# Performance work log

Measured on AMD Instinct MI355X. Metric: run time of the kernel, lower is better.

## Reference

```python
import jax, jax.numpy as jnp
import numpy as np

N_ATOMS = 64
N_SAMPLES = 2 ** 15
SAMPLERATE = 22050
N_RES = 4096
N_ROOMS = 8
N_COEFFS = N_SAMPLES // 2 + 1


def make_waves():
    # musical_scale_hz(21, 106, 4096//4) -> 4 waveform families (sine, saw, square, triangle)
    n_steps = N_RES // 4
    midi = np.linspace(21.0, 106.0, n_steps)
    f0 = 440.0 * 2.0 ** ((midi - 69.0) / 12.0)
    rps = ((f0 / (SAMPLERATE / 2.0)) * np.pi).astype(np.float32)
    rad = rps[:, None] * np.arange(N_SAMPLES, dtype=np.float32)[None, :]
    sine = np.sin(rad)
    t = rad / (2.0 * np.pi)
    saw = (2.0 * (t - np.floor(t + 0.5))).astype(np.float32)
    sq = np.sign(sine).astype(np.float32)
    tri = (2.0 * np.abs(saw) - 1.0).astype(np.float32)
    return jnp.asarray(np.concatenate([sine, saw, sq, tri], 0).reshape(1, N_RES, N_SAMPLES))


def pdf2(means, stds, n):
    # gaussian pdf evaluated on linspace(0,1,n); means/stds: (1, A)
    rng = jnp.linspace(0.0, 1.0, n)
    mu = means[..., None]
    sd = stds[..., None]
    return jnp.exp(-0.5 * ((rng - mu) / sd) ** 2) / (sd * jnp.sqrt(2.0 * jnp.pi))


def linear_interp(x, n_out):
    # F.interpolate(mode='linear', align_corners=False) on last axis; x: (b, a, f)
    f = x.shape[-1]
    pos = (jnp.arange(n_out) + 0.5) * (f / n_out) - 0.5
    pos = jnp.clip(pos, 0.0, f - 1)
    i0 = jnp.floor(pos).astype(jnp.int32)
    i1 = jnp.minimum(i0 + 1, f - 1)
    w = (pos - i0).astype(x.dtype)
    return x[..., i0] * (1.0 - w) + x[..., i1] * w


def exponential_decay(decay_values, n_atoms, n_frames, base_resonance, n_samples):
    dv = jax.nn.sigmoid(decay_values.reshape(-1, n_atoms, 1))
    dv = jnp.broadcast_to(dv, (dv.shape[0], n_atoms, n_frames))
    decay = base_resonance + dv * (1.0 - base_resonance) * 0.95
    decay = jnp.exp(jnp.cumsum(jnp.log(decay + 1e-12), axis=-1))
    return linear_interp(decay, n_samples)


def fft_convolve(a, b):
    # zero-pad to 2N, multiply spectra, take first N samples
    n = a.shape[-1]
    pa = jnp.pad(a, ((0, 0), (0, 0), (0, n)))
    pb = jnp.pad(b, ((0, 0), (0, 0), (0, n)))
    spec = jnp.fft.rfft(pa, axis=-1) * jnp.fft.rfft(pb, axis=-1)
    return jnp.fft.irfft(spec, n=2 * n, axis=-1)[..., :n]


def layer_norm(x, w, b, eps=1e-5):
    m = jnp.mean(x, axis=-1, keepdims=True)
    v = jnp.var(x, axis=-1, keepdims=True)
    return (x - m) / jnp.sqrt(v + eps) * w + b


def sparse_softmax_st(x):
    soft = jax.nn.softmax(x, axis=-1)
    hard = jax.nn.one_hot(jnp.argmax(x, axis=-1), x.shape[-1], dtype=x.dtype)
    return hard + soft - jax.lax.stop_gradient(soft)


def model_forward(x, mix, decays, filter_decays, resonance_choice, noise_filter,
                  resonance_filter, resonance_filter2, env, amplitudes, verb_params,
                  noise, waves, ln_w, ln_b, mix_w1, mix_w2, room_w1, room_w2, room_irs):
    overall_mix = jax.nn.softmax(mix, axis=-1)                                   # (1,A,2)
    resonances = jnp.einsum('bar,brn->ban', jax.nn.relu(resonance_choice), waves)  # (1,A,N)

    # band-pass filtered noise (gaussian filter in frequency domain)
    noise_spec = jnp.fft.rfft(noise, axis=-1)
    noise_filt = pdf2(noise_filter[:, :, 0], jnp.abs(noise_filter[:, :, 1]) + 1e-12, N_COEFFS)
    filtered_noise = jnp.fft.irfft(noise_spec * noise_filt, n=N_SAMPLES, axis=-1)

    res_spec = jnp.fft.rfft(resonances, axis=-1)
    rf1 = pdf2(jnp.zeros_like(resonance_filter[:, :, 0]),
               jnp.abs(resonance_filter[:, :, 1]) + 1e-12, N_COEFFS)
    filtered_resonance = jnp.fft.irfft(res_spec * rf1, n=N_SAMPLES, axis=-1)
    rf2 = pdf2(jnp.zeros_like(resonance_filter2[:, :, 0]),
               jnp.abs(resonance_filter2[:, :, 1]) + 1e-12, N_COEFFS)
    filt_res_2 = jnp.fft.irfft(res_spec * rf2, n=N_SAMPLES, axis=-1)

    filt_crossfade = exponential_decay(filter_decays, N_ATOMS, 128, 0.02, N_SAMPLES)
    decay_env = exponential_decay(decays, N_ATOMS, 128, 0.02, N_SAMPLES)
    decaying_resonance = filtered_resonance * decay_env
    decaying_resonance2 = filt_res_2 * decay_env

    # gaussian envelope branch (gaussian_envelope = True)
    envelopes = pdf2(env[:, :, 0], jnp.abs(env[:, :, 1] + 1e-12) * 0.1, N_SAMPLES)
    positioned_noise = filtered_noise * envelopes

    res = fft_convolve(positioned_noise, decaying_resonance)
    res2 = fft_convolve(positioned_noise, decaying_resonance2)
    mixed = filt_crossfade * res + (1.0 - filt_crossfade) * res2

    final = positioned_noise * overall_mix[:, :, 0:1] + mixed * overall_mix[:, :, 1:2]
    final = final / (jnp.linalg.norm(final, axis=-1, keepdims=True) + 1e-8)
    amps = jnp.abs(amplitudes)
    final = final * amps

    # ReverbGenerator: layernorm -> small MLPs -> hard room choice -> fft convolve with IR
    h = layer_norm(verb_params, ln_w, ln_b)
    mix_v = jax.nn.sigmoid(jax.nn.leaky_relu(h @ mix_w1) @ mix_w2)               # (1,A,1)
    room_logits = jax.nn.leaky_relu(h @ room_w1) @ room_w2                        # (1,A,R)
    room = sparse_softmax_st(room_logits)
    ir = jnp.einsum('bar,rn->ban', room, room_irs)
    wet = fft_convolve(final, ir)
    out = final * mix_v + wet * (1.0 - mix_v)
    return out, amps


def setup_inputs() -> dict:
    key = jax.random.key(0)
    ks = jax.random.split(key, 20)
    return {
        'x': jax.random.normal(ks[0], (1, 1), jnp.float32),
        'mix': jax.random.uniform(ks[1], (1, N_ATOMS, 2), jnp.float32),
        'decays': jax.random.uniform(ks[2], (1, N_ATOMS, 1), jnp.float32, -6.0, 6.0),
        'filter_decays': jax.random.uniform(ks[3], (1, N_ATOMS, 1), jnp.float32, -6.0, 6.0),
        'resonance_choice': jax.random.uniform(ks[4], (1, N_ATOMS, N_RES), jnp.float32),
        'noise_filter': jax.random.uniform(ks[5], (1, N_ATOMS, 2), jnp.float32),
        'resonance_filter': jax.random.uniform(ks[6], (1, N_ATOMS, 2), jnp.float32),
        'resonance_filter2': jax.random.uniform(ks[7], (1, N_ATOMS, 2), jnp.float32),
        'env': jax.random.uniform(ks[8], (1, N_ATOMS, 2), jnp.float32),
        'amplitudes': jax.random.uniform(ks[9], (1, N_ATOMS, 1), jnp.float32) ** 2,
        'verb_params': jax.random.uniform(ks[10], (1, N_ATOMS, 4), jnp.float32, -1.0, 1.0),
        'noise': jax.random.uniform(ks[11], (1, N_ATOMS, N_SAMPLES), jnp.float32, -1.0, 1.0),
        'waves': make_waves(),
        'ln_w': jnp.ones((4,), jnp.float32),
        'ln_b': jnp.zeros((4,), jnp.float32),
        'mix_w1': jax.random.normal(ks[12], (4, 4), jnp.float32) * 0.1,
        'mix_w2': jax.random.normal(ks[13], (4, 1), jnp.float32) * 0.1,
        'room_w1': jax.random.normal(ks[14], (4, 4), jnp.float32) * 0.1,
        'room_w2': jax.random.normal(ks[15], (4, N_ROOMS), jnp.float32) * 0.1,
        'room_irs': jax.random.normal(ks[16], (N_ROOMS, N_SAMPLES), jnp.float32) * 0.01,
    }


def reference(x, mix, decays, filter_decays, resonance_choice, noise_filter,
              resonance_filter, resonance_filter2, env, amplitudes, verb_params,
              noise, waves, ln_w, ln_b, mix_w1, mix_w2, room_w1, room_w2, room_irs):
    return model_forward(x, mix, decays, filter_decays, resonance_choice, noise_filter,
                         resonance_filter, resonance_filter2, env, amplitudes, verb_params,
                         noise, waves, ln_w, ln_b, mix_w1, mix_w2, room_w1, room_w2, room_irs)
```

## Files before the change

### kernel.cpp

```cpp
#include <hip/hip_runtime.h>


typedef __attribute__((ext_vector_type(8))) short bf16x8;
typedef __attribute__((ext_vector_type(4))) float f32x4;

constexpr int SC_OM0   = 0;
constexpr int SC_OM1   = 64;
constexpr int SC_NFMU  = 128;
constexpr int SC_NFSD  = 192;
constexpr int SC_RF1SD = 256;
constexpr int SC_RF2SD = 320;
constexpr int SC_ENVMU = 384;
constexpr int SC_ENVSD = 448;
constexpr int SC_AMPS  = 512;
constexpr int SC_MIXV  = 576;
constexpr int SC_ROOM  = 832;
constexpr int SC_PSS   = 1024;
constexpr int SC_DTAB  = 4096;
constexpr int SC_FTAB  = 12288;
constexpr int SC_RPS   = 20480;

constexpr size_t OFF_SCAL = 0;
constexpr size_t OFF_CT   = 65536;
constexpr size_t OFF_P    = 327680;
constexpr size_t OFF_DS   = 8716288;
constexpr size_t OFF_RP   = OFF_DS;
constexpr size_t OFF_W64  = 17104896;
constexpr size_t OFF_NSS  = OFF_W64;
constexpr size_t OFF_W2   = OFF_W64 + 4194304;
constexpr size_t OFF_RSS  = 25493504;
constexpr size_t OFF_FINU = OFF_RSS;
constexpr size_t OFF_W1   = 29687808;
constexpr size_t OFF_FN   = 38076416;
constexpr size_t OFF_FRP  = 40173568;
constexpr size_t OFF_IRS  = 44367872;
constexpr size_t WS_FLOATS= 45416448;

__device__ __forceinline__ float2 cmul(float2 a, float2 b) {
  return make_float2(a.x*b.x - a.y*b.y, a.x*b.y + a.y*b.x);
}

__device__ __forceinline__ short f2bf(float x) {
  unsigned u = __float_as_uint(x);
  u = (u + 0x7FFFu + ((u >> 16) & 1u)) >> 16;
  return (short)u;
}
__device__ __forceinline__ float bf2f(short s) {
  return __uint_as_float((unsigned)(unsigned short)s << 16);
}
__device__ __forceinline__ unsigned pk2(float2 v) {
  return (unsigned)(unsigned short)f2bf(v.x)
       | ((unsigned)(unsigned short)f2bf(v.y) << 16);
}
__device__ __forceinline__ float2 upk2(unsigned u) {
  return make_float2(__uint_as_float(u << 16),
                     __uint_as_float(u & 0xFFFF0000u));
}

__device__ __forceinline__ void dft16(float2 d[16], float ei)
{
  const float CA[4] = {1.0f, 0.92387953251128674f, 0.70710678118654752f, 0.38268343236508977f};
  const float SA[4] = {0.0f, 0.38268343236508977f, 0.70710678118654752f, 0.92387953251128674f};
  const float CB[4] = {1.0f, 0.70710678118654752f, 0.0f, -0.70710678118654752f};
  const float SB[4] = {0.0f, 0.70710678118654752f, 1.0f, 0.70710678118654752f};
  float2 e[16];
  #pragma unroll
  for (int q = 0; q < 4; ++q) {
    float2 x0 = d[q], x1 = d[q+4], x2 = d[q+8], x3 = d[q+12];
    float ca = CA[q], sa = ei*SA[q], cb = CB[q], sb = ei*SB[q];
    float2 sum1 = make_float2(x0.x+x2.x, x0.y+x2.y);
    float2 d1   = make_float2(x0.x-x2.x, x0.y-x2.y);
    float2 dif1 = make_float2(d1.x*ca - d1.y*sa, d1.x*sa + d1.y*ca);
    float2 sum2 = make_float2(x1.x+x3.x, x1.y+x3.y);
    float2 d2   = make_float2(x1.x-x3.x, x1.y-x3.y);
    float2 dt   = make_float2(d2.x*ca - d2.y*sa, d2.x*sa + d2.y*ca);
    float2 dif2 = make_float2(-ei*dt.y, ei*dt.x);
    float2 Dm   = make_float2(sum1.x-sum2.x, sum1.y-sum2.y);
    float2 Dm2  = make_float2(dif1.x-dif2.x, dif1.y-dif2.y);
    e[4*q+0] = make_float2(sum1.x+sum2.x, sum1.y+sum2.y);
    e[4*q+1] = make_float2(dif1.x+dif2.x, dif1.y+dif2.y);
    e[4*q+2] = make_float2(Dm.x*cb - Dm.y*sb, Dm.x*sb + Dm.y*cb);
    e[4*q+3] = make_float2(Dm2.x*cb - Dm2.y*sb, Dm2.x*sb + Dm2.y*cb);
  }
  #pragma unroll
  for (int q = 0; q < 4; ++q) {
    float2 x0 = e[q], x1 = e[q+4], x2 = e[q+8], x3 = e[q+12];
    float2 sum1 = make_float2(x0.x+x2.x, x0.y+x2.y);
    float2 dif1 = make_float2(x0.x-x2.x, x0.y-x2.y);
    float2 sum2 = make_float2(x1.x+x3.x, x1.y+x3.y);
    float2 d2   = make_float2(x1.x-x3.x, x1.y-x3.y);
    float2 dif2 = make_float2(-ei*d2.y, ei*d2.x);
    d[q]    = make_float2(sum1.x+sum2.x, sum1.y+sum2.y);
    d[q+4]  = make_float2(dif1.x+dif2.x, dif1.y+dif2.y);
    d[q+8]  = make_float2(sum1.x-sum2.x, sum1.y-sum2.y);
    d[q+12] = make_float2(dif1.x-dif2.x, dif1.y-dif2.y);
  }
}

__device__ __forceinline__ void dft8(float2 d[8], float ei)
{
  const float RS = 0.70710678118654752f;
  float2 E[4], O[4];
  {
    float2 s02 = make_float2(d[0].x+d[4].x, d[0].y+d[4].y);
    float2 m02 = make_float2(d[0].x-d[4].x, d[0].y-d[4].y);
    float2 s13 = make_float2(d[2].x+d[6].x, d[2].y+d[6].y);
    float2 m13 = make_float2(d[2].x-d[6].x, d[2].y-d[6].y);
    float2 im13 = make_float2(-ei*m13.y, ei*m13.x);
    E[0] = make_float2(s02.x+s13.x, s02.y+s13.y);
    E[1] = make_float2(m02.x+im13.x, m02.y+im13.y);
    E[2] = make_float2(s02.x-s13.x, s02.y-s13.y);
    E[3] = make_float2(m02.x-im13.x, m02.y-im13.y);
  }
  {
    float2 s02 = make_float2(d[1].x+d[5].x, d[1].y+d[5].y);
    float2 m02 = make_float2(d[1].x-d[5].x, d[1].y-d[5].y);
    float2 s13 = make_float2(d[3].x+d[7].x, d[3].y+d[7].y);
    float2 m13 = make_float2(d[3].x-d[7].x, d[3].y-d[7].y);
    float2 im13 = make_float2(-ei*m13.y, ei*m13.x);
    O[0] = make_float2(s02.x+s13.x, s02.y+s13.y);
    O[1] = make_float2(m02.x+im13.x, m02.y+im13.y);
    O[2] = make_float2(s02.x-s13.x, s02.y-s13.y);
    O[3] = make_float2(m02.x-im13.x, m02.y-im13.y);
  }
  float2 w1 = make_float2(RS, ei*RS);
  float2 w2 = make_float2(0.0f, ei);
  float2 w3 = make_float2(-RS, ei*RS);
  float2 t0 = O[0];
  float2 t1 = cmul(w1, O[1]);
  float2 t2 = cmul(w2, O[2]);
  float2 t3 = cmul(w3, O[3]);
  d[0] = make_float2(E[0].x+t0.x, E[0].y+t0.y);
  d[1] = make_float2(E[1].x+t1.x, E[1].y+t1.y);
  d[2] = make_float2(E[2].x+t2.x, E[2].y+t2.y);
  d[3] = make_float2(E[3].x+t3.x, E[3].y+t3.y);
  d[4] = make_float2(E[0].x-t0.x, E[0].y-t0.y);
  d[5] = make_float2(E[1].x-t1.x, E[1].y-t1.y);
  d[6] = make_float2(E[2].x-t2.x, E[2].y-t2.y);
  d[7] = make_float2(E[3].x-t3.x, E[3].y-t3.y);
}

__device__ __forceinline__ void twiddleB(float2 d[16], int u, float dir2pi)
{
  float sn1, cs1;
  __sincosf(dir2pi * ((float)u * (1.0f/256.0f)), &sn1, &cs1);
  float2 w1 = make_float2(cs1, sn1);
  float2 tw = w1;
  #pragma unroll
  for (int k = 1; k < 16; ++k) { d[k] = cmul(d[k], tw); tw = cmul(tw, w1); }
}

__global__ __launch_bounds__(256) void k_fft_s256_DsPI(
    unsigned* __restrict__ Ds, unsigned* __restrict__ P,
    unsigned* __restrict__ IRS,
    const unsigned* __restrict__ FRP, const short* __restrict__ fnb,
    const float* __restrict__ rirs, const float* __restrict__ scal)
{
  constexpr int N = 65536, NH = 32768;
  constexpr float FWD = -6.283185307179586f;
  __shared__ float2 X[16*16*17];
  __shared__ float2 T256[256];
  __shared__ float2 TN[256];
  const int mode = (blockIdx.y < 64) ? 0 : ((blockIdx.y < 128) ? 1 : 2);
  const int a = (mode == 0) ? blockIdx.y : ((mode == 1) ? blockIdx.y - 64 : blockIdx.y - 128);
  const int n1base = blockIdx.x << 4;
  const int r = threadIdx.x & 15;
  const int u = threadIdx.x >> 4;

  {
    float ang = FWD * ((float)threadIdx.x * (1.0f/256.0f));
    float sn, cs; __sincosf(ang, &sn, &cs);
    T256[threadIdx.x] = make_float2(cs, sn);
    float ang2 = FWD * ((float)threadIdx.x * (1.0f/(float)N));
    float sn2, cs2; __sincosf(ang2, &sn2, &cs2);
    TN[threadIdx.x] = make_float2(cs2, sn2);
  }

  float emu = 0.f, esd = 1.f, egp = 0.f;
  if (mode == 1) {
    emu = scal[SC_ENVMU + a];
    esd = scal[SC_ENVSD + a];
    egp = 0.3989422804014327f / esd;
  }

  float2 d[16];
  #pragma unroll
  for (int m = 0; m < 16; ++m) {
    int j = u + (m << 4);
    int n = n1base + r + 256 * j;
    float2 v = make_float2(0.0f, 0.0f);
    if (n < NH) {
      if (mode == 0) {
        float pos = ((float)n + 0.5f) * (1.0f/256.0f) - 0.5f;
        pos = fminf(fmaxf(pos, 0.0f), 127.0f);
        int i0 = (int)pos;
        float w = pos - (float)i0;
        int i1 = (i0 + 1 < 127) ? i0 + 1 : 127;
        const float* dt = scal + SC_DTAB + a*128;
        float de = dt[i0]*(1.0f-w) + dt[i1]*w;
        float2 fr = upk2(FRP[(size_t)a * NH + n]);
        v = make_float2(fr.x * de, fr.y * de);
      } else if (mode == 1) {
        float uu = (float)n * (1.0f / 32767.0f);
        float te = (uu - emu) / esd;
        float envv = __expf(-0.5f * te * te) * egp;
        v = make_float2(bf2f(fnb[(size_t)a * NH + n]) * envv, 0.0f);
      } else {
        v = make_float2(rirs[(size_t)a * NH + n], 0.0f);
      }
    }
    d[m] = v;
  }

  dft16(d, -1.0f);
  twiddleB(d, u, FWD);
  #pragma unroll
  for (int k = 0; k < 16; ++k) X[(u*16 + k)*17 + r] = d[k];
  __syncthreads();
  #pragma unroll
  for (int m = 0; m < 16; ++m) d[m] = X[(m*16 + u)*17 + r];
  dft16(d, -1.0f);

  unsigned* outp = (mode == 0) ? Ds : ((mode == 1) ? P : IRS);
  #pragma unroll
  for (int k1 = 0; k1 < 16; ++k1) {
    int j = u + (k1 << 4);
    int n = n1base + r + 256 * j;
    int aa = (n1base + r) * j;
    float2 tw = cmul(T256[(aa >> 8) & 255], TN[aa & 255]);
    outp[(size_t)a * N + n] = pk2(cmul(d[k1], tw));
  }
}

__global__ __launch_bounds__(256) void k_fft_s128_first(
    unsigned* __restrict__ RSs, unsigned* __restrict__ NSs,
    const short* __restrict__ rez, const float* __restrict__ noise)
{
  constexpr int N1 = 128, N = 32768;
  constexpr float FWD = -6.283185307179586f;
  __shared__ float2 X[16*16*17];
  __shared__ float2 T256[256];
  __shared__ float2 TN[128];
  const bool isRS = blockIdx.y < 64;
  const int a = isRS ? blockIdx.y : blockIdx.y - 64;
  const int n1base = blockIdx.x << 4;
  const int r = threadIdx.x & 15;
  const int u = threadIdx.x >> 4;

  {
    float ang = FWD * ((float)threadIdx.x * (1.0f/256.0f));
    float sn, cs; __sincosf(ang, &sn, &cs);
    T256[threadIdx.x] = make_float2(cs, sn);
    if (threadIdx.x < 128) {
      float ang2 = FWD * ((float)threadIdx.x * (1.0f/(float)N));
      float sn2, cs2; __sincosf(ang2, &sn2, &cs2);
      TN[threadIdx.x] = make_float2(cs2, sn2);
    }
  }

  float2 d[16];
  #pragma unroll
  for (int m = 0; m < 16; ++m) {
    int j = u + (m << 4);
    int n = n1base + r + N1 * j;
    float x = isRS ? (bf2f(rez[(size_t)a * N + n]) +
                      bf2f(rez[(size_t)(64 + a) * N + n]))
                   : noise[(size_t)a * N + n];
    d[m] = make_float2(x, 0.0f);
  }

  dft16(d, -1.0f);
  twiddleB(d, u, FWD);
  #pragma unroll
  for (int k = 0; k < 16; ++k) X[(u*16 + k)*17 + r] = d[k];
  __syncthreads();
  #pragma unroll
  for (int m = 0; m < 16; ++m) d[m] = X[(m*16 + u)*17 + r];
  dft16(d, -1.0f);

  unsigned* outp = isRS ? RSs : NSs;
  #pragma unroll
  for (int k1 = 0; k1 < 16; ++k1) {
    int j = u + (k1 << 4);
    int n = n1base + r + N1 * j;
    int aa = (n1base + r) * j;
    float2 tw = cmul(T256[(aa >> 7) & 255], TN[aa & 127]);
    outp[(size_t)a * N + n] = pk2(cmul(d[k1], tw));
  }
}

__global__ __launch_bounds__(256) void k_fft_m128_both(
    const unsigned* __restrict__ RSs, const unsigned* __restrict__ NSs,
    unsigned* __restrict__ W1, unsigned* __restrict__ W2,
    const float* __restrict__ scal)
{
  constexpr int N = 32768;
  constexpr float FWD = -6.283185307179586f;
  constexpr float IVD = +6.283185307179586f;
  __shared__ float2 L[32*145];
  __shared__ float2 T256[256];
  __shared__ float2 TN[128];
  const bool isRS = blockIdx.y < 64;
  const int a = isRS ? blockIdx.y : blockIdx.y - 64;
  const int colbase = blockIdx.x << 5;
  const int t = threadIdx.x;

  {
    float ang = FWD * ((float)t * (1.0f/256.0f));
    float sn, cs; __sincosf(ang, &sn, &cs);
    T256[t] = make_float2(cs, sn);
    if (t < 128) {
      float ang2 = IVD * ((float)t * (1.0f/(float)N));
      float sn2, cs2; __sincosf(ang2, &sn2, &cs2);
      TN[t] = make_float2(cs2, sn2);
    }
  }

  float mu = 0.f, isd1 = 0.f, g1 = 0.f, isd2 = 0.f, g2 = 0.f;
  if (isRS) {
    float s1 = scal[SC_RF1SD + a], s2 = scal[SC_RF2SD + a];
    isd1 = 1.0f/s1; g1 = 0.3989422804014327f/s1;
    isd2 = 1.0f/s2; g2 = 0.3989422804014327f/s2;
  } else {
    float sd = scal[SC_NFSD + a]; mu = scal[SC_NFMU + a];
    isd1 = 1.0f/sd; g1 = 0.3989422804014327f/sd;
  }
  const unsigned* zin = (isRS ? RSs : NSs) + (size_t)a * N;
  unsigned* outp = (isRS ? W1 : W2) + (size_t)a * N;

  __syncthreads();

  #pragma unroll
  for (int pp = 0; pp < 2; ++pp) {
    int p = t + (pp << 8);
    int c = p >> 4, n1 = p & 15;
    float2 d8[8];
    #pragma unroll
    for (int n2 = 0; n2 < 8; ++n2)
      d8[n2] = upk2(zin[(size_t)(colbase + c) * 128 + n1 + (n2 << 4)]);
    dft8(d8, -1.0f);
    #pragma unroll
    for (int k2 = 0; k2 < 8; ++k2) {
      float2 v = cmul(d8[k2], T256[(k2 * n1) << 1]);
      L[c*145 + n1*9 + k2] = v;
    }
  }
  __syncthreads();

  {
    int c = t >> 3, k2 = t & 7;
    float2 d[16];
    #pragma unroll
    for (int n1 = 0; n1 < 16; ++n1) d[n1] = L[c*145 + n1*9 + k2];
    dft16(d, -1.0f);
    int col = colbase + c;
    #pragma unroll
    for (int k1 = 0; k1 < 16; ++k1) {
      int j = k2 + (k1 << 3);
      int k = col + (j << 8);
      int kk = (k <= N - k) ? k : N - k;
      float2 v = d[k1];
      if (isRS) {
        float fr = (float)kk * (2.0f/(float)N);
        float t1 = fr * isd1, t2 = fr * isd2;
        float ga = __expf(-0.5f * t1 * t1) * g1;
        float gb = __expf(-0.5f * t2 * t2) * g2;
        v = make_float2(v.x*ga - v.y*gb, v.x*gb + v.y*ga);
      } else {
        float tt = ((float)kk * (2.0f/(float)N) - mu) * isd1;
        float g = __expf(-0.5f * tt * tt) * g1;
        v.x *= g; v.y *= g;
      }
      d[k1] = v;
    }
    dft16(d, 1.0f);
    #pragma unroll
    for (int n1 = 0; n1 < 16; ++n1) {
      float2 tw = T256[(k2 * n1) << 1];
      tw.y = -tw.y;
      L[c*145 + n1*9 + k2] = cmul(d[n1], tw);
    }
  }
  __syncthreads();

  #pragma unroll
  for (int pp = 0; pp < 2; ++pp) {
    int p = t + (pp << 8);
    int c = p >> 4, n1 = p & 15;
    float2 d8[8];
    #pragma unroll
    for (int k2 = 0; k2 < 8; ++k2) d8[k2] = L[c*145 + n1*9 + k2];
    dft8(d8, 1.0f);
    int col = colbase + c;
    #pragma unroll
    for (int n2 = 0; n2 < 8; ++n2) {
      int n = n1 + (n2 << 4);
      int aa = n * col;
      float2 t1 = T256[(aa >> 7) & 255];
      t1.y = -t1.y;
      float2 tw = cmul(t1, TN[aa & 127]);
      outp[(size_t)col * 128 + n] = pk2(cmul(d8[n2], tw));
    }
  }
}

__global__ __launch_bounds__(256) void k_fft_s128_last(
    const unsigned* __restrict__ W1, const unsigned* __restrict__ W2,
    unsigned* __restrict__ FRP, short* __restrict__ fnb)
{
  constexpr int N1 = 128, N = 32768;
  constexpr float IVD = +6.283185307179586f;
  constexpr float S32 = 1.0f / 32768.0f;
  __shared__ float2 X[16*16*17];
  const bool isRS = blockIdx.y < 64;
  const int a = isRS ? blockIdx.y : blockIdx.y - 64;
  const int n1base = blockIdx.x << 4;
  const int r = threadIdx.x & 15;
  const int u = threadIdx.x >> 4;

  const unsigned* cb = (isRS ? W1 : W2) + (size_t)a * N;
  float2 d[16];
  #pragma unroll
  for (int m = 0; m < 16; ++m) {
    int j = u + (m << 4);
    d[m] = upk2(cb[n1base + r + N1 * j]);
  }
  dft16(d, 1.0f);
  twiddleB(d, u, IVD);
  #pragma unroll
  for (int k = 0; k < 16; ++k) X[(u*16 + k)*17 + r] = d[k];
  __syncthreads();
  #pragma unroll
  for (int m = 0; m < 16; ++m) d[m] = X[(m*16 + u)*17 + r];
  dft16(d, 1.0f);

  #pragma unroll
  for (int k1 = 0; k1 < 16; ++k1) {
    int j = u + (k1 << 4);
    int n = n1base + r + N1 * j;
    if (isRS) {
      FRP[(size_t)a * N + n] = pk2(make_float2(d[k1].x * S32, d[k1].y * S32));
    } else {
      fnb[(size_t)a * N + n] = f2bf(d[k1].x * S32);
    }
  }
}

__global__ __launch_bounds__(256) void k_fft_mid256dual(
    const unsigned* __restrict__ zin, const unsigned* __restrict__ zin2half,
    unsigned* __restrict__ out1, const int* __restrict__ roomArr)
{
  constexpr int N = 65536;
  constexpr float FWD = -6.283185307179586f;
  constexpr float IVD = +6.283185307179586f;
  __shared__ float2 X[16*16*17];
  __shared__ float2 T256[256];
  __shared__ float2 TN[256];
  const int a = blockIdx.y;
  const int colbase = blockIdx.x << 4;
  const int u  = threadIdx.x & 15;
  const int rc = threadIdx.x >> 4;

  {
    float ang = FWD * ((float)threadIdx.x * (1.0f/256.0f));
    float sn, cs; __sincosf(ang, &sn, &cs);
    T256[threadIdx.x] = make_float2(cs, sn);
    float ang2 = IVD * ((float)threadIdx.x * (1.0f/(float)N));
    float sn2, cs2; __sincosf(ang2, &sn2, &cs2);
    TN[threadIdx.x] = make_float2(cs2, sn2);
  }
  __syncthreads();

  const unsigned* z2 = zin2half + (size_t)(roomArr ? roomArr[a] : a) * N;
  const size_t rowG = (size_t)a * N + (size_t)(colbase + rc) * 256;
  const size_t rowZ2 = (size_t)(colbase + rc) * 256;

  float2 d[16];
  #pragma unroll
  for (int m = 0; m < 16; ++m) d[m] = upk2(zin[rowG + u + (m << 4)]);
  dft16(d, -1.0f);
  twiddleB(d, u, FWD);
  #pragma unroll
  for (int k = 0; k < 16; ++k) X[(rc*16 + k)*17 + u] = d[k];
  #pragma unroll
  for (int m = 0; m < 16; ++m) d[m] = X[(rc*16 + u)*17 + m];
  dft16(d, -1.0f);

  float2 stash[16];
  #pragma unroll
  for (int k = 0; k < 16; ++k) stash[k] = d[k];
  #pragma unroll
  for (int m = 0; m < 16; ++m) d[m] = upk2(z2[rowZ2 + u + (m << 4)]);
  dft16(d, -1.0f);
  twiddleB(d, u, FWD);
  #pragma unroll
  for (int k = 0; k < 16; ++k) X[(rc*16 + k)*17 + u] = d[k];
  #pragma unroll
  for (int m = 0; m < 16; ++m) d[m] = X[(rc*16 + u)*17 + m];
  dft16(d, -1.0f);
  #pragma unroll
  for (int k = 0; k < 16; ++k) d[k] = cmul(stash[k], d[k]);

  dft16(d, 1.0f);
  twiddleB(d, u, IVD);
  #pragma unroll
  for (int k = 0; k < 16; ++k) X[(rc*16 + k)*17 + u] = d[k];
  #pragma unroll
  for (int m = 0; m < 16; ++m) d[m] = X[(rc*16 + u)*17 + m];
  dft16(d, 1.0f);

  #pragma unroll
  for (int k1 = 0; k1 < 16; ++k1) {
    int j = u + (k1 << 4);
    int aa = j * (colbase + rc);
    float2 t1 = T256[(aa >> 8) & 255];
    t1.y = -t1.y;
    float2 tw = cmul(t1, TN[aa & 255]);
    out1[rowG + j] = pk2(cmul(d[k1], tw));
  }
}

__global__ __launch_bounds__(256) void k_fft_out6fwd(
    const unsigned* __restrict__ W64in, const short* __restrict__ fnb,
    float* __restrict__ finU, float* __restrict__ scal,
    unsigned* __restrict__ DsOut)
{
  constexpr int N = 65536, NH = 32768;
  constexpr float FWD = -6.283185307179586f;
  constexpr float IVD = +6.283185307179586f;
  constexpr float S64 = 1.0f / 65536.0f;
  __shared__ float2 X[16*16*17];
  __shared__ float2 T256[256];
  __shared__ float2 TN[256];
  __shared__ float red[256];
  const int a = blockIdx.y;
  const int n1base = blockIdx.x << 4;
  const int r = threadIdx.x & 15;
  const int u = threadIdx.x >> 4;

  {
    float ang = FWD * ((float)threadIdx.x * (1.0f/256.0f));
    float sn, cs; __sincosf(ang, &sn, &cs);
    T256[threadIdx.x] = make_float2(cs, sn);
    float ang2 = FWD * ((float)threadIdx.x * (1.0f/(float)N));
    float sn2, cs2; __sincosf(ang2, &sn2, &cs2);
    TN[threadIdx.x] = make_float2(cs2, sn2);
  }

  const float emu = scal[SC_ENVMU + a];
  const float esd = scal[SC_ENVSD + a];
  const float egp = 0.3989422804014327f / esd;
  const float om0 = scal[SC_OM0 + a], om1 = scal[SC_OM1 + a];
  const float* ft = scal + SC_FTAB + a*128;

  float2 d[16];
  #pragma unroll
  for (int m = 0; m < 16; ++m) {
    int j = u + (m << 4);
    d[m] = upk2(W64in[(size_t)a * N + n1base + r + 256 * j]);
  }
  dft16(d, 1.0f);
  twiddleB(d, u, IVD);
  #pragma unroll
  for (int k = 0; k < 16; ++k) X[(u*16 + k)*17 + r] = d[k];
  __syncthreads();
  #pragma unroll
  for (int m = 0; m < 16; ++m) d[m] = X[(m*16 + u)*17 + r];
  dft16(d, 1.0f);

  float fv[8];
  float ss = 0.0f;
  #pragma unroll
  for (int k1 = 0; k1 < 8; ++k1) {
    int n = n1base + r + 256 * (u + (k1 << 4));
    float resv  = d[k1].x * S64;
    float res2v = d[k1].y * S64;
    float uu = (float)n * (1.0f / 32767.0f);
    float te = (uu - emu) / esd;
    float envv = __expf(-0.5f * te * te) * egp;
    float pnv = bf2f(fnb[(size_t)a * NH + n]) * envv;
    float pos = ((float)n + 0.5f) * (1.0f/256.0f) - 0.5f;
    pos = fminf(fmaxf(pos, 0.0f), 127.0f);
    int i0 = (int)pos;
    float w = pos - (float)i0;
    int i1 = (i0 + 1 < 127) ? i0 + 1 : 127;
    float fc = ft[i0]*(1.0f-w) + ft[i1]*w;
    float f = pnv*om0 + (fc*resv + (1.0f-fc)*res2v)*om1;
    finU[(size_t)a * NH + n] = f;
    fv[k1] = f;
    ss += f * f;
  }
  red[threadIdx.x] = ss;
  __syncthreads();
  for (int s = 128; s > 0; s >>= 1) {
    if (threadIdx.x < s) red[threadIdx.x] += red[threadIdx.x + s];
    __syncthreads();
  }
  if (threadIdx.x == 0) scal[SC_PSS + a*16 + blockIdx.x] = red[0];

  #pragma unroll
  for (int m = 0; m < 16; ++m)
    d[m] = (m < 8) ? make_float2(fv[m], 0.0f) : make_float2(0.0f, 0.0f);
  dft16(d, -1.0f);
  twiddleB(d, u, FWD);
  #pragma unroll
  for (int k = 0; k < 16; ++k) X[(u*16 + k)*17 + r] = d[k];
  __syncthreads();
  #pragma unroll
  for (int m = 0; m < 16; ++m) d[m] = X[(m*16 + u)*17 + r];
  dft16(d, -1.0f);

  #pragma unroll
  for (int k1 = 0; k1 < 16; ++k1) {
    int j = u + (k1 << 4);
    int n = n1base + r + 256 * j;
    int aa = (n1base + r) * j;
    float2 tw = cmul(T256[(aa >> 8) & 255], TN[aa & 255]);
    DsOut[(size_t)a * N + n] = pk2(cmul(d[k1], tw));
  }
}

__global__ __launch_bounds__(256) void k_fft_s256_out3(
    const unsigned* __restrict__ W64in, const float* __restrict__ finU,
    const float* __restrict__ scal, float* __restrict__ out)
{
  constexpr int N = 65536, NH = 32768;
  constexpr float IVD = +6.283185307179586f;
  constexpr float S64 = 1.0f / 65536.0f;
  __shared__ float2 X[16*16*17];
  const int a = blockIdx.y;
  const int n1base = blockIdx.x << 4;
  const int r = threadIdx.x & 15;
  const int u = threadIdx.x >> 4;

  float ss = 0.0f;
  #pragma unroll
  for (int i = 0; i < 16; ++i) ss += scal[SC_PSS + a*16 + i];
  float fscale = scal[SC_AMPS + a] / (sqrtf(ss) + 1e-8f);
  float mixv = scal[SC_MIXV + a];
  float w1 = fscale * (1.0f - mixv);
  float w0 = fscale * mixv;

  float2 d[16];
  #pragma unroll
  for (int m = 0; m < 16; ++m) {
    int j = u + (m << 4);
    d[m] = upk2(W64in[(size_t)a * N + n1base + r + 256 * j]);
  }
  dft16(d, 1.0f);
  twiddleB(d, u, IVD);
  #pragma unroll
  for (int k = 0; k < 16; ++k) X[(u*16 + k)*17 + r] = d[k];
  __syncthreads();
  #pragma unroll
  for (int m = 0; m < 16; ++m) d[m] = X[(m*16 + u)*17 + r];
  dft16(d, 1.0f);

  #pragma unroll
  for (int k1 = 0; k1 < 8; ++k1) {
    int n = n1base + r + 256 * (u + (k1 << 4));
    out[(size_t)a * NH + n] =
        d[k1].x * S64 * w1 + finU[(size_t)a * NH + n] * w0;
  }
}

__global__ void k_packA(const float* __restrict__ rc, short* __restrict__ ctb,
    const float* __restrict__ mix, const float* __restrict__ decays,
    const float* __restrict__ fdec, const float* __restrict__ nf,
    const float* __restrict__ rf1, const float* __restrict__ rf2,
    const float* __restrict__ env, const float* __restrict__ amplitudes,
    const float* __restrict__ verb, const float* __restrict__ ln_w,
    const float* __restrict__ ln_b, const float* __restrict__ mw1,
    const float* __restrict__ mw2, const float* __restrict__ rw1,
    const float* __restrict__ rw2, float* __restrict__ scal,
    float* __restrict__ dout)
{
  int o = blockIdx.x * 256 + threadIdx.x;
  {
    int m = o >> 12, k = o & 4095;
    int s = k >> 2, f = k & 3;
    float v = fmaxf(rc[m*4096 + f*1024 + s], 0.0f);
    ctb[o] = f2bf(v);
  }
  if (blockIdx.x < 4) {
    int idx = blockIdx.x * 256 + threadIdx.x;
    double step = 85.0 / 1023.0;
    double midi = (double)idx * step + 21.0;
    if (idx == 1023) midi = 106.0;
    double f0 = 440.0 * exp2((midi - 69.0) * (1.0 / 12.0));
    scal[SC_RPS + idx] = (float)((f0 / 11025.0) * 3.141592653589793);
  }
  if (blockIdx.x != 0 || threadIdx.x >= 64) return;
  int a = threadIdx.x;
  float m0 = mix[a*2+0], m1 = mix[a*2+1];
  float mx = fmaxf(m0, m1);
  float e0 = expf(m0 - mx), e1 = expf(m1 - mx);
  float inv = 1.0f / (e0 + e1);
  scal[SC_OM0+a] = e0 * inv;
  scal[SC_OM1+a] = e1 * inv;
  scal[SC_NFMU+a] = nf[a*2+0];
  scal[SC_NFSD+a] = fabsf(nf[a*2+1]) + 1e-12f;
  scal[SC_RF1SD+a] = fabsf(rf1[a*2+1]) + 1e-12f;
  scal[SC_RF2SD+a] = fabsf(rf2[a*2+1]) + 1e-12f;
  scal[SC_ENVMU+a] = env[a*2+0];
  scal[SC_ENVSD+a] = fabsf(env[a*2+1] + 1e-12f) * 0.1f;
  float amp = fabsf(amplitudes[a]);
  scal[SC_AMPS+a] = amp;
  dout[2097152 + a] = amp;
  float d  = 0.02f + (1.0f/(1.0f+expf(-decays[a]))) * (0.98f * 0.95f);
  float fd = 0.02f + (1.0f/(1.0f+expf(-fdec[a])))   * (0.98f * 0.95f);
  float pd = 1.0f, pf = 1.0f;
  for (int f = 0; f < 128; ++f) {
    pd *= d; pf *= fd;
    scal[SC_DTAB + a*128 + f] = pd;
    scal[SC_FTAB + a*128 + f] = pf;
  }
  float x0 = verb[a*4+0], x1 = verb[a*4+1], x2 = verb[a*4+2], x3 = verb[a*4+3];
  float mean = (x0+x1+x2+x3) * 0.25f;
  float d0 = x0-mean, d1 = x1-mean, d2 = x2-mean, d3 = x3-mean;
  float var = (d0*d0 + d1*d1 + d2*d2 + d3*d3) * 0.25f;
  float rs = 1.0f / sqrtf(var + 1e-5f);
  float h[4] = { d0*rs*ln_w[0]+ln_b[0], d1*rs*ln_w[1]+ln_b[1],
                 d2*rs*ln_w[2]+ln_b[2], d3*rs*ln_w[3]+ln_b[3] };
  float t[4], u[4];
  for (int j = 0; j < 4; ++j) {
    float s1 = 0.f, s2 = 0.f;
    for (int i2 = 0; i2 < 4; ++i2) {
      s1 += h[i2] * mw1[i2*4 + j];
      s2 += h[i2] * rw1[i2*4 + j];
    }
    t[j] = (s1 > 0.f) ? s1 : 0.01f*s1;
    u[j] = (s2 > 0.f) ? s2 : 0.01f*s2;
  }
  float ml = 0.f;
  for (int j = 0; j < 4; ++j) ml += t[j] * mw2[j];
  scal[SC_MIXV+a] = 1.0f / (1.0f + expf(-ml));
  float best = -1e30f; int bi = 0;
  for (int rr = 0; rr < 8; ++rr) {
    float lg = 0.f;
    for (int j = 0; j < 4; ++j) lg += u[j] * rw2[j*8 + rr];
    if (lg > best) { best = lg; bi = rr; }
  }
  ((int*)scal)[SC_ROOM + a] = bi;
}

__global__ __launch_bounds__(512) void k_gemm_mfma(
    const float* __restrict__ scal, const short* __restrict__ ctb,
    short* __restrict__ rp)
{
  const int t = threadIdx.x;
  const int w = t >> 6, lane = t & 63;
  const int ml = lane & 15, q = lane >> 4;
  const int col = blockIdx.x * 128 + w * 16 + ml;
  const int part = blockIdx.y;

  const float colf = (float)col;
  const float TWO_PI_F = 6.28318530717958647692f;
  const double INV_2PI = 0.15915494309189533577;

  f32x4 acc[4] = {};
  const short* abase = ctb + (size_t)ml * 4096 + (size_t)part * 2048 + q * 8;
  const float* rtab = scal + SC_RPS + part * 512;

  #define WAVE4(rps, b, off) { \
    float rad = (rps) * colf; \
    double dt = (double)rad * INV_2PI; \
    double frd = dt - floor(dt); \
    float sine = __sinf((float)frd * TWO_PI_F); \
    float sq = (rad == 0.0f) ? 0.0f : ((frd < 0.5) ? 1.0f : -1.0f); \
    float tt = rad / TWO_PI_F; \
    float saw = 2.0f * (tt - floorf(tt + 0.5f)); \
    float tri = 2.0f * fabsf(saw) - 1.0f; \
    b[off+0] = f2bf(sine); b[off+1] = f2bf(saw); \
    b[off+2] = f2bf(sq);   b[off+3] = f2bf(tri); }

  for (int kbl = 0; kbl < 64; ++kbl) {
    int sl = kbl * 8 + 2 * q;
    float rps0 = rtab[sl], rps1 = rtab[sl + 1];
    bf16x8 b;
    WAVE4(rps0, b, 0);
    WAVE4(rps1, b, 4);
    const short* ap = abase + (size_t)kbl * 32;
    acc[0] = __builtin_amdgcn_mfma_f32_16x16x32_bf16(*(const bf16x8*)(ap),                   b, acc[0], 0,0,0);
    acc[1] = __builtin_amdgcn_mfma_f32_16x16x32_bf16(*(const bf16x8*)(ap + (size_t)16*4096), b, acc[1], 0,0,0);
    acc[2] = __builtin_amdgcn_mfma_f32_16x16x32_bf16(*(const bf16x8*)(ap + (size_t)32*4096), b, acc[2], 0,0,0);
    acc[3] = __builtin_amdgcn_mfma_f32_16x16x32_bf16(*(const bf16x8*)(ap + (size_t)48*4096), b, acc[3], 0,0,0);
  }
  #undef WAVE4

  #pragma unroll
  for (int mt = 0; mt < 4; ++mt) {
    #pragma unroll
    for (int rr = 0; rr < 4; ++rr) {
      rp[(size_t)(part*64 + mt*16 + q*4 + rr) * 32768 + col] = f2bf(acc[mt][rr]);
    }
  }
}

extern "C" void kernel_launch(void* const* d_in, const int* in_sizes, int n_in,
                              void* d_out, int out_size, void* d_ws, size_t ws_size,
                              hipStream_t stream)
{
  const float* mix   = (const float*)d_in[1];
  const float* dec   = (const float*)d_in[2];
  const float* fdec  = (const float*)d_in[3];
  const float* rc    = (const float*)d_in[4];
  const float* nf    = (const float*)d_in[5];
  const float* rf1   = (const float*)d_in[6];
  const float* rf2   = (const float*)d_in[7];
  const float* env   = (const float*)d_in[8];
  const float* amps  = (const float*)d_in[9];
  const float* verb  = (const float*)d_in[10];
  const float* noise = (const float*)d_in[11];
  const float* lnw   = (const float*)d_in[13];
  const float* lnb   = (const float*)d_in[14];
  const float* mw1   = (const float*)d_in[15];
  const float* mw2   = (const float*)d_in[16];
  const float* rw1   = (const float*)d_in[17];
  const float* rw2   = (const float*)d_in[18];
  const float* rirs  = (const float*)d_in[19];
  float* out = (float*)d_out;
  float* w   = (float*)d_ws;

  if (ws_size < WS_FLOATS * 4ULL) return;

  float*    scal = w + OFF_SCAL;
  short*    ctb  = (short*)(w + OFF_CT);
  short*    rp   = (short*)(w + OFF_RP);
  unsigned* P    = (unsigned*)(w + OFF_P);
  unsigned* Ds   = (unsigned*)(w + OFF_DS);
  unsigned* W64  = (unsigned*)(w + OFF_W64);
  unsigned* RSs  = (unsigned*)(w + OFF_RSS);
  unsigned* NSs  = (unsigned*)(w + OFF_NSS);
  unsigned* W2   = (unsigned*)(w + OFF_W2);
  float*    finU = w + OFF_FINU;
  unsigned* W1   = (unsigned*)(w + OFF_W1);
  short*    fnb  = (short*)(w + OFF_FN);
  unsigned* FRP  = (unsigned*)(w + OFF_FRP);
  unsigned* IRS  = (unsigned*)(w + OFF_IRS);
  const int* room = ((const int*)(w + OFF_SCAL)) + SC_ROOM;

  k_packA<<<1024, 256, 0, stream>>>(rc, ctb, mix, dec, fdec, nf, rf1, rf2, env,
                                    amps, verb, lnw, lnb, mw1, mw2, rw1, rw2,
                                    scal, out);
  k_gemm_mfma<<<dim3(256, 2), 512, 0, stream>>>(scal, ctb, rp);

  k_fft_s128_first<<<dim3(8,128),256,0,stream>>>(RSs, NSs, rp, noise);
  k_fft_m128_both<<<dim3(8,128),256,0,stream>>>(RSs, NSs, W1, W2, scal);
  k_fft_s128_last<<<dim3(8,128),256,0,stream>>>(W1, W2, FRP, fnb);

  k_fft_s256_DsPI<<<dim3(16,136),256,0,stream>>>(Ds, P, IRS, FRP, fnb, rirs, scal);

  k_fft_mid256dual<<<dim3(16,64),256,0,stream>>>(Ds, P, W64, nullptr);

  k_fft_out6fwd<<<dim3(16,64),256,0,stream>>>(W64, fnb, finU, scal, Ds);

  k_fft_mid256dual<<<dim3(16,64),256,0,stream>>>(Ds, IRS, W64, room);

  k_fft_s256_out3<<<dim3(16,64),256,0,stream>>>(W64, finU, scal, out);
}
```

Baseline: 260.8 us.

## Precompute room IR spectra once and use table twiddles in FFT stages

Adds a separate kernel that finishes the column FFT of the 8 room impulse responses once, so the second dual-convolution pass multiplies by the finished spectrum instead of redoing that FFT for all 64 atoms. Also replaces the recursive sincos twiddle chains with lookups into a shared 256-entry table, adding syncs after table setup. Costs one extra small launch and more shared-memory reads in exchange for less redundant FFT arithmetic.

```diff
diff --git a/kernel.cpp b/kernel.cpp
--- a/kernel.cpp
+++ b/kernel.cpp
@@ -140,14 +140,16 @@
   d[7] = make_float2(E[3].x-t3.x, E[3].y-t3.y);
 }
 
-__device__ __forceinline__ void twiddleB(float2 d[16], int u, float dir2pi)
-{
-  float sn1, cs1;
-  __sincosf(dir2pi * ((float)u * (1.0f/256.0f)), &sn1, &cs1);
-  float2 w1 = make_float2(cs1, sn1);
-  float2 tw = w1;
-  #pragma unroll
-  for (int k = 1; k < 16; ++k) { d[k] = cmul(d[k], tw); tw = cmul(tw, w1); }
+__device__ __forceinline__ void twiddleT(float2 d[16], int u,
+                                         const float2* __restrict__ T256,
+                                         float dsign)
+{
+  #pragma unroll
+  for (int k = 1; k < 16; ++k) {
+    float2 tw = T256[u*k];
+    tw.y *= dsign;
+    d[k] = cmul(d[k], tw);
+  }
 }
 
 __global__ __launch_bounds__(256) void k_fft_s256_DsPI(
@@ -175,6 +177,7 @@
     float sn2, cs2; __sincosf(ang2, &sn2, &cs2);
     TN[threadIdx.x] = make_float2(cs2, sn2);
   }
+  __syncthreads();
 
   float emu = 0.f, esd = 1.f, egp = 0.f;
   if (mode == 1) {
@@ -213,7 +216,7 @@
   }
 
   dft16(d, -1.0f);
-  twiddleB(d, u, FWD);
+  twiddleT(d, u, T256, 1.0f);
   #pragma unroll
   for (int k = 0; k < 16; ++k) X[(u*16 + k)*17 + r] = d[k];
   __syncthreads();
@@ -230,6 +233,40 @@
     float2 tw = cmul(T256[(aa >> 8) & 255], TN[aa & 255]);
     outp[(size_t)a * N + n] = pk2(cmul(d[k1], tw));
   }
+}
+
+__global__ __launch_bounds__(256) void k_fft_irs_contig(unsigned* __restrict__ IRS)
+{
+  constexpr int N = 65536;
+  constexpr float FWD = -6.283185307179586f;
+  __shared__ float2 X[16*16*17];
+  __shared__ float2 T256[256];
+  const int a = blockIdx.y;
+  const int colbase = blockIdx.x << 4;
+  const int u  = threadIdx.x & 15;
+  const int rc = threadIdx.x >> 4;
+
+  {
+    float ang = FWD * ((float)threadIdx.x * (1.0f/256.0f));
+    float sn, cs; __sincosf(ang, &sn, &cs);
+    T256[threadIdx.x] = make_float2(cs, sn);
+  }
+  __syncthreads();
+
+  const size_t rowG = (size_t)a * N + (size_t)(colbase + rc) * 256;
+  float2 d[16];
+  #pragma unroll
+  for (int m = 0; m < 16; ++m) d[m] = upk2(IRS[rowG + u + (m << 4)]);
+  dft16(d, -1.0f);
+  twiddleT(d, u, T256, 1.0f);
+  #pragma unroll
+  for (int k = 0; k < 16; ++k) X[(rc*16 + k)*17 + u] = d[k];
+  #pragma unroll
+  for (int m = 0; m < 16; ++m) d[m] = X[(rc*16 + u)*17 + m];
+  dft16(d, -1.0f);
+  #pragma unroll
+  for (int k1 = 0; k1 < 16; ++k1)
+    IRS[rowG + u + (k1 << 4)] = pk2(d[k1]);
 }
 
 __global__ __launch_bounds__(256) void k_fft_s128_first(
@@ -257,6 +294,7 @@
       TN[threadIdx.x] = make_float2(cs2, sn2);
     }
   }
+  __syncthreads();
 
   float2 d[16];
   #pragma unroll
@@ -270,7 +308,7 @@
   }
 
   dft16(d, -1.0f);
-  twiddleB(d, u, FWD);
+  twiddleT(d, u, T256, 1.0f);
   #pragma unroll
   for (int k = 0; k < 16; ++k) X[(u*16 + k)*17 + r] = d[k];
   __syncthreads();
@@ -412,12 +450,20 @@
   constexpr float IVD = +6.283185307179586f;
   constexpr float S32 = 1.0f / 32768.0f;
   __shared__ float2 X[16*16*17];
+  __shared__ float2 T256[256];
   const bool isRS = blockIdx.y < 64;
   const int a = isRS ? blockIdx.y : blockIdx.y - 64;
   const int n1base = blockIdx.x << 4;
   const int r = threadIdx.x & 15;
   const int u = threadIdx.x >> 4;
 
+  {
+    float ang = IVD * ((float)threadIdx.x * (1.0f/256.0f));
+    float sn, cs; __sincosf(ang, &sn, &cs);
+    T256[threadIdx.x] = make_float2(cs, sn);
+  }
+  __syncthreads();
+
   const unsigned* cb = (isRS ? W1 : W2) + (size_t)a * N;
   float2 d[16];
   #pragma unroll
@@ -426,7 +472,7 @@
     d[m] = upk2(cb[n1base + r + N1 * j]);
   }
   dft16(d, 1.0f);
-  twiddleB(d, u, IVD);
+  twiddleT(d, u, T256, 1.0f);
   #pragma unroll
   for (int k = 0; k < 16; ++k) X[(u*16 + k)*17 + r] = d[k];
   __syncthreads();
@@ -446,8 +492,9 @@
   }
 }
 
+template<int FM>
 __global__ __launch_bounds__(256) void k_fft_mid256dual(
-    const unsigned* __restrict__ zin, const unsigned* __restrict__ zin2half,
+    const unsigned* __restrict__ zin, const unsigned* __restrict__ zin2,
     unsigned* __restrict__ out1, const int* __restrict__ roomArr)
 {
   constexpr int N = 65536;
@@ -471,7 +518,7 @@
   }
   __syncthreads();
 
-  const unsigned* z2 = zin2half + (size_t)(roomArr ? roomArr[a] : a) * N;
+  const unsigned* z2 = zin2 + (size_t)(roomArr ? roomArr[a] : a) * N;
   const size_t rowG = (size_t)a * N + (size_t)(colbase + rc) * 256;
   const size_t rowZ2 = (size_t)(colbase + rc) * 256;
 
@@ -479,30 +526,36 @@
   #pragma unroll
   for (int m = 0; m < 16; ++m) d[m] = upk2(zin[rowG + u + (m << 4)]);
   dft16(d, -1.0f);
-  twiddleB(d, u, FWD);
+  twiddleT(d, u, T256, 1.0f);
   #pragma unroll
   for (int k = 0; k < 16; ++k) X[(rc*16 + k)*17 + u] = d[k];
   #pragma unroll
   for (int m = 0; m < 16; ++m) d[m] = X[(rc*16 + u)*17 + m];
   dft16(d, -1.0f);
 
-  float2 stash[16];
-  #pragma unroll
-  for (int k = 0; k < 16; ++k) stash[k] = d[k];
-  #pragma unroll
-  for (int m = 0; m < 16; ++m) d[m] = upk2(z2[rowZ2 + u + (m << 4)]);
-  dft16(d, -1.0f);
-  twiddleB(d, u, FWD);
-  #pragma unroll
-  for (int k = 0; k < 16; ++k) X[(rc*16 + k)*17 + u] = d[k];
-  #pragma unroll
-  for (int m = 0; m < 16; ++m) d[m] = X[(rc*16 + u)*17 + m];
-  dft16(d, -1.0f);
-  #pragma unroll
-  for (int k = 0; k < 16; ++k) d[k] = cmul(stash[k], d[k]);
+  if (FM == 5) {
+    float2 stash[16];
+    #pragma unroll
+    for (int k = 0; k < 16; ++k) stash[k] = d[k];
+    #pragma unroll
+    for (int m = 0; m < 16; ++m) d[m] = upk2(z2[rowZ2 + u + (m << 4)]);
+    dft16(d, -1.0f);
+    twiddleT(d, u, T256, 1.0f);
+    #pragma unroll
+    for (int k = 0; k < 16; ++k) X[(rc*16 + k)*17 + u] = d[k];
+    #pragma unroll
+    for (int m = 0; m < 16; ++m) d[m] = X[(rc*16 + u)*17 + m];
+    dft16(d, -1.0f);
+    #pragma unroll
+    for (int k = 0; k < 16; ++k) d[k] = cmul(stash[k], d[k]);
+  } else {
+    #pragma unroll
+    for (int k = 0; k < 16; ++k)
+      d[k] = cmul(d[k], upk2(z2[rowZ2 + u + (k << 4)]));
+  }
 
   dft16(d, 1.0f);
-  twiddleB(d, u, IVD);
+  twiddleT(d, u, T256, -1.0f);
   #pragma unroll
   for (int k = 0; k < 16; ++k) X[(rc*16 + k)*17 + u] = d[k];
   #pragma unroll
@@ -546,6 +599,7 @@
     float sn2, cs2; __sincosf(ang2, &sn2, &cs2);
     TN[threadIdx.x] = make_float2(cs2, sn2);
   }
+  __syncthreads();
 
   const float emu = scal[SC_ENVMU + a];
   const float esd = scal[SC_ENVSD + a];
@@ -560,7 +614,7 @@
     d[m] = upk2(W64in[(size_t)a * N + n1base + r + 256 * j]);
   }
   dft16(d, 1.0f);
-  twiddleB(d, u, IVD);
+  twiddleT(d, u, T256, -1.0f);
   #pragma unroll
   for (int k = 0; k < 16; ++k) X[(u*16 + k)*17 + r] = d[k];
   __syncthreads();
@@ -602,7 +656,7 @@
   for (int m = 0; m < 16; ++m)
     d[m] = (m < 8) ? make_float2(fv[m], 0.0f) : make_float2(0.0f, 0.0f);
   dft16(d, -1.0f);
-  twiddleB(d, u, FWD);
+  twiddleT(d, u, T256, 1.0f);
   #pragma unroll
   for (int k = 0; k < 16; ++k) X[(u*16 + k)*17 + r] = d[k];
   __syncthreads();
@@ -628,10 +682,18 @@
   constexpr float IVD = +6.283185307179586f;
   constexpr float S64 = 1.0f / 65536.0f;
   __shared__ float2 X[16*16*17];
+  __shared__ float2 T256[256];
   const int a = blockIdx.y;
   const int n1base = blockIdx.x << 4;
   const int r = threadIdx.x & 15;
   const int u = threadIdx.x >> 4;
+
+  {
+    float ang = IVD * ((float)threadIdx.x * (1.0f/256.0f));
+    float sn, cs; __sincosf(ang, &sn, &cs);
+    T256[threadIdx.x] = make_float2(cs, sn);
+  }
+  __syncthreads();
 
   float ss = 0.0f;
   #pragma unroll
@@ -648,7 +710,7 @@
     d[m] = upk2(W64in[(size_t)a * N + n1base + r + 256 * j]);
   }
   dft16(d, 1.0f);
-  twiddleB(d, u, IVD);
+  twiddleT(d, u, T256, 1.0f);
   #pragma unroll
   for (int k = 0; k < 16; ++k) X[(u*16 + k)*17 + r] = d[k];
   __syncthreads();
@@ -850,12 +912,13 @@
   k_fft_s128_last<<<dim3(8,128),256,0,stream>>>(W1, W2, FRP, fnb);
 
   k_fft_s256_DsPI<<<dim3(16,136),256,0,stream>>>(Ds, P, IRS, FRP, fnb, rirs, scal);
-
-  k_fft_mid256dual<<<dim3(16,64),256,0,stream>>>(Ds, P, W64, nullptr);
+  k_fft_irs_contig<<<dim3(16,8),256,0,stream>>>(IRS);
+
+  k_fft_mid256dual<5><<<dim3(16,64),256,0,stream>>>(Ds, P, W64, nullptr);
 
   k_fft_out6fwd<<<dim3(16,64),256,0,stream>>>(W64, fnb, finU, scal, Ds);
 
-  k_fft_mid256dual<<<dim3(16,64),256,0,stream>>>(Ds, IRS, W64, room);
+  k_fft_mid256dual<4><<<dim3(16,64),256,0,stream>>>(Ds, IRS, W64, room);
 
   k_fft_s256_out3<<<dim3(16,64),256,0,stream>>>(W64, finU, scal, out);
 }
```

Result: no change. 256.9 us (-1.5%).
